# Optimization experiments

Measured on AMD Instinct MI355X. Metric: run time of the kernel, lower is better.

The kernel has to match this reference:

```python
import jax, jax.numpy as jnp
import numpy as np

B = 32          # num graphs
N = 4096        # nodes per graph (temporal length after reshape)
TOT = B * N     # 131072 total nodes
F = 64          # num_features
HS = 128        # hidden_dim_s
RS = 32         # rank_s
HT = 128        # hidden_dim_t
RT = 32         # rank_t
E = 1048576     # num edges


def setup_inputs() -> dict:
    key = jax.random.key(0)
    ks = jax.random.split(key, 20)
    x = jax.random.normal(ks[0], (TOT, F), jnp.float32)
    edge_index = jax.random.randint(ks[1], (2, E), 0, TOT, dtype=jnp.int64)
    batch = jnp.repeat(jnp.arange(B, dtype=jnp.int64), N)

    def lin(k, fan_in, fan_out):
        s = 1.0 / np.sqrt(fan_in)
        return jax.random.uniform(k, (fan_in, fan_out), jnp.float32, -s, s)

    def conv(k, cout, cin):
        s = 1.0 / np.sqrt(cin * 3)
        return jax.random.uniform(k, (cout, cin, 3), jnp.float32, -s, s)

    return {
        "x": x, "edge_index": edge_index, "batch": batch,
        "W1": lin(ks[2], F, HS), "b1": jnp.zeros((HS,), jnp.float32),
        "W2": lin(ks[3], HS, RS), "b2": jnp.zeros((RS,), jnp.float32),
        "W3": lin(ks[4], RS, HS), "b3": jnp.zeros((HS,), jnp.float32),
        "tW1": conv(ks[5], HT, HS), "tb1": jnp.zeros((HT,), jnp.float32),
        "tW2": conv(ks[6], RT, HT), "tb2": jnp.zeros((RT,), jnp.float32),
        "tW3": conv(ks[7], HT, RT), "tb3": jnp.zeros((HT,), jnp.float32),
        "Wpi": lin(ks[8], HT, 1), "bpi": jnp.zeros((1,), jnp.float32),
        "Wn": lin(ks[9], HT, 1), "bn": jnp.zeros((1,), jnp.float32),
        "Wp": lin(ks[10], HT, 1), "bp": jnp.zeros((1,), jnp.float32),
    }


def reference(x, edge_index, batch,
              W1, b1, W2, b2, W3, b3,
              tW1, tb1, tW2, tb2, tW3, tb3,
              Wpi, bpi, Wn, bn, Wp, bp):
    src, dst = edge_index[0], edge_index[1]
    n = x.shape[0]

    # GCN symmetric normalization with added self-loops (PyG GCNConv default)
    deg = jnp.zeros((n,), x.dtype).at[dst].add(1.0) + 1.0  # +1 self-loop
    dinv = jax.lax.rsqrt(deg)
    enorm = dinv[src] * dinv[dst]       # [E] edge normalization
    snorm = dinv * dinv                 # [n] self-loop normalization

    def gcn(h, W, b):
        h = h @ W                                            # [n, out]
        agg = jnp.zeros_like(h).at[dst].add(h[src] * enorm[:, None])
        return agg + h * snorm[:, None] + b

    xs = jax.nn.relu(gcn(x, W1, b1))
    xs = jax.nn.relu(gcn(xs, W2, b2))
    xs = jax.nn.relu(gcn(xs, W3, b3))    # [TOT, HS]

    num_graphs = B  # == batch.max() + 1 (batch is repeat(arange(B), N))
    xs = xs.reshape(num_graphs, -1, xs.shape[-1]).transpose(0, 2, 1)  # [B, HS, N]

    def conv1d(z, w, bias):
        y = jax.lax.conv_general_dilated(
            z, w, window_strides=(1,), padding=((1, 1),),
            dimension_numbers=("NCH", "OIH", "NCH"))
        return y + bias[None, :, None]

    xt = jax.nn.relu(conv1d(xs, tW1, tb1))
    xt = jax.nn.relu(conv1d(xt, tW2, tb2))
    xt = jax.nn.relu(conv1d(xt, tW3, tb3))                   # [B, HT, N]

    xt = xt.transpose(0, 2, 1).reshape(-1, xt.shape[1])      # [TOT, HT]

    pi = jax.nn.sigmoid(xt @ Wpi + bpi)
    nb = jax.nn.softplus(xt @ Wn + bn)
    p = jax.nn.sigmoid(xt @ Wp + bp)
    return (pi, nb, p)
```

## Files before the change

kernel.cpp:

```cpp
#include <hip/hip_runtime.h>
#include <cmath>

constexpr int TOT = 131072;
constexpr int NE  = 1048576;
constexpr int NMASK = 4095;

constexpr int NB   = 512;
constexpr int DPB  = 256;
constexpr int BCAP = 4096;
constexpr int EPB  = 2048;

typedef __attribute__((ext_vector_type(8))) short bf16x8;
typedef __attribute__((ext_vector_type(4))) float f32x4;

__device__ inline float bf2f(unsigned int u16) {
    union { unsigned int i; float f; } x; x.i = u16 << 16; return x.f;
}
__device__ inline unsigned short f2bf(float f) {
    union { float f; unsigned int i; } x; x.f = f;
    unsigned int r = (x.i + 0x7fffu + ((x.i >> 16) & 1u)) >> 16;
    return (unsigned short)r;
}
__device__ inline void unpack8(uint4 v, float* f) {
    f[0] = bf2f(v.x & 0xffffu); f[1] = bf2f(v.x >> 16);
    f[2] = bf2f(v.y & 0xffffu); f[3] = bf2f(v.y >> 16);
    f[4] = bf2f(v.z & 0xffffu); f[5] = bf2f(v.z >> 16);
    f[6] = bf2f(v.w & 0xffffu); f[7] = bf2f(v.w >> 16);
}
__device__ inline uint4 pack8(const float* f) {
    uint4 v;
    v.x = (unsigned)f2bf(f[0]) | ((unsigned)f2bf(f[1]) << 16);
    v.y = (unsigned)f2bf(f[2]) | ((unsigned)f2bf(f[3]) << 16);
    v.z = (unsigned)f2bf(f[4]) | ((unsigned)f2bf(f[5]) << 16);
    v.w = (unsigned)f2bf(f[6]) | ((unsigned)f2bf(f[7]) << 16);
    return v;
}

__global__ __launch_bounds__(256) void k_part(const int* __restrict__ src,
                                              const int* __restrict__ dst,
                                              int* __restrict__ gcur,
                                              unsigned* __restrict__ buf) {
    __shared__ int hist[NB];
    __shared__ int cbase[NB];
    __shared__ int lcur[NB];
    const int tid = threadIdx.x;
    const int e0 = blockIdx.x * EPB;

    for (int b = tid; b < NB; b += 256) hist[b] = 0;
    __syncthreads();
    for (int i = tid; i < EPB; i += 256)
        atomicAdd(&hist[dst[e0 + i] >> 8], 1);
    __syncthreads();
    for (int b = tid; b < NB; b += 256) {
        int c = hist[b];
        cbase[b] = (c > 0) ? atomicAdd(&gcur[b * 32], c) : 0;
        lcur[b] = 0;
    }
    __syncthreads();
    for (int i = tid; i < EPB; i += 256) {
        int e = e0 + i;
        int d = dst[e];
        int b = d >> 8;
        int p = atomicAdd(&lcur[b], 1);
        buf[b * BCAP + cbase[b] + p] = ((unsigned)src[e] << 8) | (unsigned)(d & 255);
    }
}

__global__ __launch_bounds__(256) void k_bcsr(const unsigned* __restrict__ buf,
                                              const int* __restrict__ gcur,
                                              int* __restrict__ adj,
                                              int2* __restrict__ rse,
                                              float* __restrict__ dinv) {
    __shared__ int cnt[DPB];
    __shared__ int start[DPB];
    __shared__ int cur[DPB];
    __shared__ int sc[DPB];
    const int b = blockIdx.x;
    const int tid = threadIdx.x;
    cnt[tid] = 0;
    __syncthreads();
    const int n = gcur[b * 32];
    const unsigned* eb = buf + b * BCAP;
    for (int i = tid; i < n; i += 256)
        atomicAdd(&cnt[eb[i] & 255u], 1);
    __syncthreads();
    int v = cnt[tid];
    sc[tid] = v;
    __syncthreads();
    for (int off = 1; off < 256; off <<= 1) {
        int a = sc[tid];
        int p = (tid >= off) ? sc[tid - off] : 0;
        __syncthreads();
        sc[tid] = a + p;
        __syncthreads();
    }
    int st = sc[tid] - v;
    start[tid] = st;
    cur[tid] = 0;
    int d = (b << 8) + tid;
    rse[d] = make_int2(b * BCAP + st, v);
    dinv[d] = rsqrtf((float)v + 1.0f);
    __syncthreads();
    for (int i = tid; i < n; i += 256) {
        unsigned w = eb[i];
        int dl = (int)(w & 255u);
        int p = atomicAdd(&cur[dl], 1);
        adj[b * BCAP + start[dl] + p] = (int)(w >> 8);
    }
}

__global__ __launch_bounds__(256) void k_packall(
    const float* __restrict__ W1, const float* __restrict__ W2, const float* __restrict__ W3,
    const float* __restrict__ tW1, const float* __restrict__ tW2, const float* __restrict__ tW3,
    unsigned short* __restrict__ g1, unsigned short* __restrict__ g2, unsigned short* __restrict__ g3,
    unsigned short* __restrict__ c1, unsigned short* __restrict__ c2, unsigned short* __restrict__ c3) {
    int gid = blockIdx.x * 256 + threadIdx.x;
    const float* w; unsigned short* wp; int CIN, COUT, taps, idx;
    if      (gid <  8192) { w = W1;  wp = g1; CIN = 64;  COUT = 128; taps = 1; idx = gid; }
    else if (gid < 12288) { w = W2;  wp = g2; CIN = 128; COUT = 32;  taps = 1; idx = gid - 8192; }
    else if (gid < 16384) { w = W3;  wp = g3; CIN = 32;  COUT = 128; taps = 1; idx = gid - 12288; }
    else if (gid < 65536) { w = tW1; wp = c1; CIN = 128; COUT = 128; taps = 3; idx = gid - 16384; }
    else if (gid < 77824) { w = tW2; wp = c2; CIN = 128; COUT = 32;  taps = 3; idx = gid - 65536; }
    else if (gid < 90112) { w = tW3; wp = c3; CIN = 32;  COUT = 128; taps = 3; idx = gid - 77824; }
    else return;
    int j = idx & 7;
    int L = (idx >> 3) & 63;
    int f = idx >> 9;
    int NT = COUT >> 4;
    int kc = f / NT, nt = f - kc * NT;
    int k = kc * 32 + (L >> 4) * 8 + j;
    int n = nt * 16 + (L & 15);
    float v;
    if (taps == 1) v = w[k * COUT + n];
    else { int t = k / CIN, c = k - t * CIN; v = w[(n * CIN + c) * 3 + t]; }
    wp[idx] = f2bf(v);
}

__global__ __launch_bounds__(256) void k_scale64b(const float4* __restrict__ x,
                                                  const float* __restrict__ dinv,
                                                  uint4* __restrict__ out) {
    int t = blockIdx.x * 256 + threadIdx.x;
    int row = t >> 3;
    float d = dinv[row];
    float4 v0 = x[t * 2], v1 = x[t * 2 + 1];
    float f[8] = { v0.x * d, v0.y * d, v0.z * d, v0.w * d,
                   v1.x * d, v1.y * d, v1.z * d, v1.w * d };
    out[t] = pack8(f);
}

template<int LC>
__global__ __launch_bounds__(256) void k_gcsr(const uint4* __restrict__ xs,
                                              const int* __restrict__ adj,
                                              const int2* __restrict__ rse,
                                              const float* __restrict__ dinv,
                                              const float* __restrict__ bias,
                                              uint4* __restrict__ out) {
    int t = blockIdx.x * 256 + threadIdx.x;
    int d = t >> LC;
    int g = t & ((1 << LC) - 1);
    float a[8];
    unpack8(xs[t], a);
    int2 se = rse[d];
    int e = se.x, end = se.x + se.y;
    for (; e + 4 <= end; e += 4) {
        int s0 = adj[e], s1 = adj[e + 1], s2 = adj[e + 2], s3 = adj[e + 3];
        uint4 v0 = xs[(s0 << LC) + g];
        uint4 v1 = xs[(s1 << LC) + g];
        uint4 v2 = xs[(s2 << LC) + g];
        uint4 v3 = xs[(s3 << LC) + g];
        float f[8];
        unpack8(v0, f);
#pragma unroll
        for (int j = 0; j < 8; ++j) a[j] += f[j];
        unpack8(v1, f);
#pragma unroll
        for (int j = 0; j < 8; ++j) a[j] += f[j];
        unpack8(v2, f);
#pragma unroll
        for (int j = 0; j < 8; ++j) a[j] += f[j];
        unpack8(v3, f);
#pragma unroll
        for (int j = 0; j < 8; ++j) a[j] += f[j];
    }
    for (; e < end; ++e) {
        float f[8];
        unpack8(xs[(adj[e] << LC) + g], f);
#pragma unroll
        for (int j = 0; j < 8; ++j) a[j] += f[j];
    }
    float dv = dinv[d];
#pragma unroll
    for (int j = 0; j < 8; ++j)
        a[j] = fmaxf(fmaf(a[j], dv, bias[g * 8 + j]), 0.0f) * dv;
    out[t] = pack8(a);
}

template<int CIN, bool RELU>
__global__ __launch_bounds__(256) void k_gmm(const uint4* __restrict__ xs,
                                             const int* __restrict__ adj,
                                             const int2* __restrict__ rse,
                                             const float* __restrict__ dinv,
                                             const bf16x8* __restrict__ wp,
                                             const float* __restrict__ bias,
                                             unsigned short* __restrict__ y) {
    constexpr int COUT = 128;
    constexpr int ROWS = 64;
    constexpr int SC = CIN + 8;
    constexpr int NV = CIN / 8;
    constexpr int VPT = NV / 4;
    constexpr int NK = CIN / 32;
    constexpr int NT = COUT / 16;
    constexpr int WN = 2, WM = 4;
    __shared__ __attribute__((aligned(16))) unsigned short tile[ROWS * SC];

    const int R0 = blockIdx.x * ROWS;
    const int tid = threadIdx.x;

    {
        int r = R0 + (tid >> 2);
        int g = tid & 3;
        const uint4* base = xs + (long)r * NV + g * VPT;
        float a[VPT * 8];
#pragma unroll
        for (int v = 0; v < VPT; ++v) unpack8(base[v], a + v * 8);
        int2 se = rse[r];
        int e = se.x, end = se.x + se.y;
        for (; e + 2 <= end; e += 2) {
            int s0 = adj[e], s1 = adj[e + 1];
            const uint4* p0 = xs + (long)s0 * NV + g * VPT;
            const uint4* p1 = xs + (long)s1 * NV + g * VPT;
            uint4 v0[VPT], v1[VPT];
#pragma unroll
            for (int v = 0; v < VPT; ++v) { v0[v] = p0[v]; v1[v] = p1[v]; }
            float f[VPT * 8];
#pragma unroll
            for (int v = 0; v < VPT; ++v) unpack8(v0[v], f + v * 8);
#pragma unroll
            for (int j = 0; j < VPT * 8; ++j) a[j] += f[j];
#pragma unroll
            for (int v = 0; v < VPT; ++v) unpack8(v1[v], f + v * 8);
#pragma unroll
            for (int j = 0; j < VPT * 8; ++j) a[j] += f[j];
        }
        for (; e < end; ++e) {
            const uint4* p0 = xs + (long)adj[e] * NV + g * VPT;
            float f[VPT * 8];
#pragma unroll
            for (int v = 0; v < VPT; ++v) unpack8(p0[v], f + v * 8);
#pragma unroll
            for (int j = 0; j < VPT * 8; ++j) a[j] += f[j];
        }
        float dv = dinv[r];
#pragma unroll
        for (int j = 0; j < VPT * 8; ++j) a[j] *= dv;
        uint4* dst4 = (uint4*)(tile + (tid >> 2) * SC + g * VPT * 8);
#pragma unroll
        for (int v = 0; v < VPT; ++v) dst4[v] = pack8(a + v * 8);
    }
    __syncthreads();

    const int lane = threadIdx.x & 63;
    const int w = threadIdx.x >> 6;
    const int l16 = lane & 15;
    const int q = lane >> 4;
    const int colbase = w * 32;
    const int nt0 = colbase >> 4;

    f32x4 acc[WM][WN];
#pragma unroll
    for (int wm = 0; wm < WM; ++wm)
#pragma unroll
        for (int nt = 0; nt < WN; ++nt) acc[wm][nt] = (f32x4){0.f, 0.f, 0.f, 0.f};

    const bf16x8* __restrict__ wpl = wp + lane;

#pragma unroll
    for (int kc = 0; kc < NK; ++kc) {
        bf16x8 a[WM];
#pragma unroll
        for (int wm = 0; wm < WM; ++wm)
            a[wm] = *(const bf16x8*)(tile + (wm * 16 + l16) * SC + kc * 32 + q * 8);
        bf16x8 b[WN];
#pragma unroll
        for (int nt = 0; nt < WN; ++nt)
            b[nt] = wpl[(kc * NT + nt0 + nt) * 64];
#pragma unroll
        for (int wm = 0; wm < WM; ++wm)
#pragma unroll
            for (int nt = 0; nt < WN; ++nt)
                acc[wm][nt] = __builtin_amdgcn_mfma_f32_16x16x32_bf16(a[wm], b[nt], acc[wm][nt], 0, 0, 0);
    }

#pragma unroll
    for (int wm = 0; wm < WM; ++wm) {
#pragma unroll
        for (int nt = 0; nt < WN; ++nt) {
            int col = colbase + nt * 16 + l16;
            float bi = bias[col];
#pragma unroll
            for (int r = 0; r < 4; ++r) {
                int row = R0 + wm * 16 + q * 4 + r;
                float v = acc[wm][nt][r] + bi;
                if (RELU) v = fmaxf(v, 0.0f);
                y[(long)row * COUT + col] = f2bf(v);
            }
        }
    }
}

template<int CIN, int COUT, int TAPS, bool RELU, bool BIAS, bool SOUT>
__global__ __launch_bounds__(256) void k_mm(const unsigned short* __restrict__ x,
                                            const bf16x8* __restrict__ wp,
                                            const float* __restrict__ bias,
                                            const float* __restrict__ dinv,
                                            unsigned short* __restrict__ y) {
    constexpr int ROWS = 64;
    constexpr int HALO = (TAPS == 3) ? 1 : 0;
    constexpr int TR = ROWS + 2 * HALO;
    constexpr int SC = CIN + 8;
    constexpr int NCH = CIN / 32;
    constexpr int NK = TAPS * NCH;
    constexpr int NT = COUT / 16;
    constexpr int WN = (COUT == 128) ? 2 : 1;
    constexpr int WM = (COUT == 128) ? 4 : 2;
    __shared__ __attribute__((aligned(16))) unsigned short tile[TR * SC];

    const int R0 = blockIdx.x * ROWS;
    const int n0 = R0 & NMASK; (void)n0;

    constexpr int NLD = TR * (CIN / 8);
    for (int idx = threadIdx.x; idx < NLD; idx += 256) {
        int tr = idx / (CIN / 8);
        int c8 = idx - tr * (CIN / 8);
        int ro = tr - HALO;
        bool valid = true;
        if (TAPS == 3) {
            if (ro < 0) valid = (n0 > 0);
            else if (ro >= ROWS) valid = (n0 + ROWS < 4096);
        }
        uint4 v = make_uint4(0, 0, 0, 0);
        if (valid) v = *(const uint4*)(x + (long)(R0 + ro) * CIN + c8 * 8);
        *(uint4*)(tile + tr * SC + c8 * 8) = v;
    }
    __syncthreads();

    const int lane = threadIdx.x & 63;
    const int w = threadIdx.x >> 6;
    const int l16 = lane & 15;
    const int q = lane >> 4;
    const int colbase = (COUT == 128) ? w * 32 : (w & 1) * 16;
    const int rowbase = (COUT == 128) ? 0 : (w >> 1) * 32;
    const int nt0 = colbase >> 4;

    f32x4 acc[WM][WN];
#pragma unroll
    for (int wm = 0; wm < WM; ++wm)
#pragma unroll
        for (int nt = 0; nt < WN; ++nt) acc[wm][nt] = (f32x4){0.f, 0.f, 0.f, 0.f};

    const bf16x8* __restrict__ wpl = wp + lane;

#pragma unroll
    for (int kc = 0; kc < NK; ++kc) {
        const int tap = (TAPS == 3) ? (kc / NCH) : 0;
        const int ch  = (TAPS == 3) ? (kc - tap * NCH) : kc;
        bf16x8 a[WM];
#pragma unroll
        for (int wm = 0; wm < WM; ++wm)
            a[wm] = *(const bf16x8*)(tile + (rowbase + wm * 16 + l16 + tap) * SC + ch * 32 + q * 8);
        bf16x8 b[WN];
#pragma unroll
        for (int nt = 0; nt < WN; ++nt)
            b[nt] = wpl[(kc * NT + nt0 + nt) * 64];
#pragma unroll
        for (int wm = 0; wm < WM; ++wm)
#pragma unroll
            for (int nt = 0; nt < WN; ++nt)
                acc[wm][nt] = __builtin_amdgcn_mfma_f32_16x16x32_bf16(a[wm], b[nt], acc[wm][nt], 0, 0, 0);
    }

#pragma unroll
    for (int wm = 0; wm < WM; ++wm) {
#pragma unroll
        for (int nt = 0; nt < WN; ++nt) {
            int col = colbase + nt * 16 + l16;
            float bi = BIAS ? bias[col] : 0.0f;
#pragma unroll
            for (int r = 0; r < 4; ++r) {
                int row = R0 + rowbase + wm * 16 + q * 4 + r;
                float v = acc[wm][nt][r] + bi;
                if (RELU) v = fmaxf(v, 0.0f);
                if (SOUT) v *= dinv[row];
                y[(long)row * COUT + col] = f2bf(v);
            }
        }
    }
}

__global__ __launch_bounds__(256) void k_conv_heads(
    const unsigned short* __restrict__ x, const bf16x8* __restrict__ wp,
    const float* __restrict__ bias,
    const float* __restrict__ Wpi, const float* __restrict__ bpi,
    const float* __restrict__ Wn,  const float* __restrict__ bn,
    const float* __restrict__ Wp,  const float* __restrict__ bp,
    float* __restrict__ out) {
    constexpr int CIN = 32;
    constexpr int ROWS = 64, HALO = 1, TR = 66, SC = CIN + 8;
    constexpr int NK = 3, NT = 8, WN = 2, WM = 4;
    __shared__ __attribute__((aligned(16))) unsigned short tile[TR * SC];
    __shared__ unsigned short xts[64 * 130];

    const int R0 = blockIdx.x * ROWS;
    const int n0 = R0 & NMASK;

    constexpr int NLD = TR * (CIN / 8);
    for (int idx = threadIdx.x; idx < NLD; idx += 256) {
        int tr = idx / (CIN / 8);
        int c8 = idx - tr * (CIN / 8);
        int ro = tr - HALO;
        bool valid = true;
        if (ro < 0) valid = (n0 > 0);
        else if (ro >= ROWS) valid = (n0 + ROWS < 4096);
        uint4 v = make_uint4(0, 0, 0, 0);
        if (valid) v = *(const uint4*)(x + (long)(R0 + ro) * CIN + c8 * 8);
        *(uint4*)(tile + tr * SC + c8 * 8) = v;
    }
    __syncthreads();

    const int lane = threadIdx.x & 63;
    const int w = threadIdx.x >> 6;
    const int l16 = lane & 15;
    const int q = lane >> 4;
    const int colbase = w * 32;
    const int nt0 = colbase >> 4;

    f32x4 acc[WM][WN];
#pragma unroll
    for (int wm = 0; wm < WM; ++wm)
#pragma unroll
        for (int nt = 0; nt < WN; ++nt) acc[wm][nt] = (f32x4){0.f, 0.f, 0.f, 0.f};

    const bf16x8* __restrict__ wpl = wp + lane;

#pragma unroll
    for (int kc = 0; kc < NK; ++kc) {
        bf16x8 a[WM];
#pragma unroll
        for (int wm = 0; wm < WM; ++wm)
            a[wm] = *(const bf16x8*)(tile + (wm * 16 + l16 + kc) * SC + q * 8);
        bf16x8 b[WN];
#pragma unroll
        for (int nt = 0; nt < WN; ++nt)
            b[nt] = wpl[(kc * NT + nt0 + nt) * 64];
#pragma unroll
        for (int wm = 0; wm < WM; ++wm)
#pragma unroll
            for (int nt = 0; nt < WN; ++nt)
                acc[wm][nt] = __builtin_amdgcn_mfma_f32_16x16x32_bf16(a[wm], b[nt], acc[wm][nt], 0, 0, 0);
    }

#pragma unroll
    for (int wm = 0; wm < WM; ++wm) {
#pragma unroll
        for (int nt = 0; nt < WN; ++nt) {
            int col = colbase + nt * 16 + l16;
            float bi = bias[col];
#pragma unroll
            for (int r = 0; r < 4; ++r) {
                int row = wm * 16 + q * 4 + r;
                xts[row * 130 + col] = f2bf(fmaxf(acc[wm][nt][r] + bi, 0.0f));
            }
        }
    }
    __syncthreads();
    if (threadIdx.x < 192) {
        int h = threadIdx.x >> 6;
        int row = threadIdx.x & 63;
        const float* Wh = (h == 0) ? Wpi : (h == 1) ? Wn : Wp;
        float s = 0.0f;
        const unsigned short* xr = xts + row * 130;
#pragma unroll
        for (int c2 = 0; c2 < 64; ++c2) {
            unsigned u = *(const unsigned*)(xr + c2 * 2);
            s = fmaf(bf2f(u & 0xffffu), Wh[c2 * 2], s);
            s = fmaf(bf2f(u >> 16), Wh[c2 * 2 + 1], s);
        }
        float bb = (h == 0) ? bpi[0] : (h == 1) ? bn[0] : bp[0];
        float z = s + bb;
        float o;
        if (h == 1) o = (z > 20.0f) ? z : log1pf(expf(z));
        else        o = 1.0f / (1.0f + expf(-z));
        out[h * TOT + R0 + row] = o;
    }
}

extern "C" void kernel_launch(void* const* d_in, const int* in_sizes, int n_in,
                              void* d_out, int out_size, void* d_ws, size_t ws_size,
                              hipStream_t stream) {
    const float* x   = (const float*)d_in[0];
    const int*   ei  = (const int*)d_in[1];
    const int*   src = ei;
    const int*   dst = ei + NE;
    const float* W1 = (const float*)d_in[3];
    const float* b1 = (const float*)d_in[4];
    const float* W2 = (const float*)d_in[5];
    const float* b2 = (const float*)d_in[6];
    const float* W3 = (const float*)d_in[7];
    const float* b3 = (const float*)d_in[8];
    const float* tW1 = (const float*)d_in[9];
    const float* tb1 = (const float*)d_in[10];
    const float* tW2 = (const float*)d_in[11];
    const float* tb2 = (const float*)d_in[12];
    const float* tW3 = (const float*)d_in[13];
    const float* tb3 = (const float*)d_in[14];
    const float* Wpi = (const float*)d_in[15];
    const float* bpi = (const float*)d_in[16];
    const float* Wn  = (const float*)d_in[17];
    const float* bn  = (const float*)d_in[18];
    const float* Wp  = (const float*)d_in[19];
    const float* bp  = (const float*)d_in[20];

    char* ws = (char*)d_ws;
    float* dinv = (float*)(ws + (0ull << 20));
    int*   gcur = (int*)  (ws + (1ull << 20));
    int2*  rse  = (int2*) (ws + (1ull << 20) + (256 << 10));
    unsigned short* wpG1 = (unsigned short*)(ws + (3ull << 20));
    unsigned short* wpG2 = (unsigned short*)(ws + (3ull << 20) + (128 << 10));
    unsigned short* wpG3 = (unsigned short*)(ws + (3ull << 20) + (256 << 10));
    unsigned short* wpC1 = (unsigned short*)(ws + (3ull << 20) + (384 << 10));
    unsigned short* wpC2 = (unsigned short*)(ws + (3ull << 20) + (512 << 10));
    unsigned short* wpC3 = (unsigned short*)(ws + (3ull << 20) + (640 << 10));
    unsigned* buf = (unsigned*)(ws + (4ull << 20));
    int* adj = (int*)(ws + (12ull << 20));
    unsigned short* Xa = (unsigned short*)(ws + (24ull  << 20));
    unsigned short* Xb = (unsigned short*)(ws + (44ull  << 20));
    unsigned short* Xc = (unsigned short*)(ws + (80ull  << 20));
    unsigned short* Xd = (unsigned short*)(ws + (116ull << 20));
    unsigned short* Xe = (unsigned short*)(ws + (128ull << 20));

    hipMemsetAsync(gcur, 0, NB * 32 * sizeof(int), stream);
    k_packall<<<352, 256, 0, stream>>>(W1, W2, W3, tW1, tW2, tW3,
                                       wpG1, wpG2, wpG3, wpC1, wpC2, wpC3);

    k_part<<<NE / EPB, 256, 0, stream>>>(src, dst, gcur, buf);
    k_bcsr<<<NB, 256, 0, stream>>>(buf, gcur, adj, rse, dinv);

    k_scale64b<<<TOT * 8 / 256, 256, 0, stream>>>((const float4*)x, dinv, (uint4*)Xa);
    k_gmm<64, true><<<TOT / 64, 256, 0, stream>>>((const uint4*)Xa, adj, rse, dinv,
                                                  (const bf16x8*)wpG1, b1, Xc);

    k_mm<128, 32, 1, false, false, true>
        <<<TOT / 64, 256, 0, stream>>>(Xc, (const bf16x8*)wpG2, nullptr, dinv, Xd);
    k_gcsr<2><<<TOT * 4 / 256, 256, 0, stream>>>((const uint4*)Xd, adj, rse, dinv,
                                                 b2, (uint4*)Xe);

    k_gmm<32, true><<<TOT / 64, 256, 0, stream>>>((const uint4*)Xe, adj, rse, dinv,
                                                  (const bf16x8*)wpG3, b3, Xb);

    k_mm<128, 128, 3, true, true, false>
        <<<TOT / 64, 256, 0, stream>>>(Xb, (const bf16x8*)wpC1, tb1, nullptr, Xc);
    k_mm<128, 32, 3, true, true, false>
        <<<TOT / 64, 256, 0, stream>>>(Xc, (const bf16x8*)wpC2, tb2, nullptr, Xd);

    k_conv_heads<<<TOT / 64, 256, 0, stream>>>(Xd, (const bf16x8*)wpC3, tb3,
                                               Wpi, bpi, Wn, bn, Wp, bp, (float*)d_out);
}
```

Measured before the change: 286.7 us.

## Fuse three temporal convs and heads into one halo-recompute kernel

Merges the three temporal conv1d layers and the output heads into a single kernel. Each block loads a 64-row tile with a 3-row halo and recomputes the halo rows of the intermediate layers in shared memory, so the intermediate activations are never written to or read from global memory. It also folds the input scaling into the CSR-build kernel to remove one launch, and unrolls the GCN gather loop by four. The cost is redundant halo compute, much larger shared memory per block (lower occupancy), and higher register pressure.

After: 288.0 us. About the same (+0.5%).

```diff
diff --git a/kernel.cpp b/kernel.cpp
--- a/kernel.cpp
+++ b/kernel.cpp
@@ -70,7 +70,9 @@
                                               const int* __restrict__ gcur,
                                               int* __restrict__ adj,
                                               int2* __restrict__ rse,
-                                              float* __restrict__ dinv) {
+                                              float* __restrict__ dinv,
+                                              const float4* __restrict__ x,
+                                              uint4* __restrict__ xsc) {
     __shared__ int cnt[DPB];
     __shared__ int start[DPB];
     __shared__ int cur[DPB];
@@ -106,6 +108,15 @@
         int dl = (int)(w & 255u);
         int p = atomicAdd(&cur[dl], 1);
         adj[b * BCAP + start[dl] + p] = (int)(w >> 8);
+    }
+    for (int i = tid; i < DPB * 8; i += 256) {
+        int rl = i >> 3;
+        int t = (b << 11) + i;
+        float dv = rsqrtf((float)cnt[rl] + 1.0f);
+        float4 v0 = x[t * 2], v1 = x[t * 2 + 1];
+        float f[8] = { v0.x * dv, v0.y * dv, v0.z * dv, v0.w * dv,
+                       v1.x * dv, v1.y * dv, v1.z * dv, v1.w * dv };
+        xsc[t] = pack8(f);
     }
 }
 
@@ -136,18 +147,6 @@
     wp[idx] = f2bf(v);
 }
 
-__global__ __launch_bounds__(256) void k_scale64b(const float4* __restrict__ x,
-                                                  const float* __restrict__ dinv,
-                                                  uint4* __restrict__ out) {
-    int t = blockIdx.x * 256 + threadIdx.x;
-    int row = t >> 3;
-    float d = dinv[row];
-    float4 v0 = x[t * 2], v1 = x[t * 2 + 1];
-    float f[8] = { v0.x * d, v0.y * d, v0.z * d, v0.w * d,
-                   v1.x * d, v1.y * d, v1.z * d, v1.w * d };
-    out[t] = pack8(f);
-}
-
 template<int LC>
 __global__ __launch_bounds__(256) void k_gcsr(const uint4* __restrict__ xs,
                                               const int* __restrict__ adj,
@@ -225,13 +224,15 @@
         for (int v = 0; v < VPT; ++v) unpack8(base[v], a + v * 8);
         int2 se = rse[r];
         int e = se.x, end = se.x + se.y;
-        for (; e + 2 <= end; e += 2) {
-            int s0 = adj[e], s1 = adj[e + 1];
+        for (; e + 4 <= end; e += 4) {
+            int s0 = adj[e], s1 = adj[e + 1], s2 = adj[e + 2], s3 = adj[e + 3];
             const uint4* p0 = xs + (long)s0 * NV + g * VPT;
             const uint4* p1 = xs + (long)s1 * NV + g * VPT;
-            uint4 v0[VPT], v1[VPT];
-#pragma unroll
-            for (int v = 0; v < VPT; ++v) { v0[v] = p0[v]; v1[v] = p1[v]; }
+            const uint4* p2 = xs + (long)s2 * NV + g * VPT;
+            const uint4* p3 = xs + (long)s3 * NV + g * VPT;
+            uint4 v0[VPT], v1[VPT], v2[VPT], v3[VPT];
+#pragma unroll
+            for (int v = 0; v < VPT; ++v) { v0[v] = p0[v]; v1[v] = p1[v]; v2[v] = p2[v]; v3[v] = p3[v]; }
             float f[VPT * 8];
 #pragma unroll
             for (int v = 0; v < VPT; ++v) unpack8(v0[v], f + v * 8);
@@ -239,6 +240,14 @@
             for (int j = 0; j < VPT * 8; ++j) a[j] += f[j];
 #pragma unroll
             for (int v = 0; v < VPT; ++v) unpack8(v1[v], f + v * 8);
+#pragma unroll
+            for (int j = 0; j < VPT * 8; ++j) a[j] += f[j];
+#pragma unroll
+            for (int v = 0; v < VPT; ++v) unpack8(v2[v], f + v * 8);
+#pragma unroll
+            for (int j = 0; j < VPT * 8; ++j) a[j] += f[j];
+#pragma unroll
+            for (int v = 0; v < VPT; ++v) unpack8(v3[v], f + v * 8);
 #pragma unroll
             for (int j = 0; j < VPT * 8; ++j) a[j] += f[j];
         }
@@ -308,38 +317,25 @@
     }
 }
 
-template<int CIN, int COUT, int TAPS, bool RELU, bool BIAS, bool SOUT>
+template<int CIN, int COUT, bool SOUT>
 __global__ __launch_bounds__(256) void k_mm(const unsigned short* __restrict__ x,
                                             const bf16x8* __restrict__ wp,
-                                            const float* __restrict__ bias,
                                             const float* __restrict__ dinv,
                                             unsigned short* __restrict__ y) {
     constexpr int ROWS = 64;
-    constexpr int HALO = (TAPS == 3) ? 1 : 0;
-    constexpr int TR = ROWS + 2 * HALO;
     constexpr int SC = CIN + 8;
-    constexpr int NCH = CIN / 32;
-    constexpr int NK = TAPS * NCH;
+    constexpr int NK = CIN / 32;
     constexpr int NT = COUT / 16;
-    constexpr int WN = (COUT == 128) ? 2 : 1;
-    constexpr int WM = (COUT == 128) ? 4 : 2;
-    __shared__ __attribute__((aligned(16))) unsigned short tile[TR * SC];
+    constexpr int WN = 1, WM = 2;
+    __shared__ __attribute__((aligned(16))) unsigned short tile[ROWS * SC];
 
     const int R0 = blockIdx.x * ROWS;
-    const int n0 = R0 & NMASK; (void)n0;
-
-    constexpr int NLD = TR * (CIN / 8);
+
+    constexpr int NLD = ROWS * (CIN / 8);
     for (int idx = threadIdx.x; idx < NLD; idx += 256) {
         int tr = idx / (CIN / 8);
         int c8 = idx - tr * (CIN / 8);
-        int ro = tr - HALO;
-        bool valid = true;
-        if (TAPS == 3) {
-            if (ro < 0) valid = (n0 > 0);
-            else if (ro >= ROWS) valid = (n0 + ROWS < 4096);
-        }
-        uint4 v = make_uint4(0, 0, 0, 0);
-        if (valid) v = *(const uint4*)(x + (long)(R0 + ro) * CIN + c8 * 8);
+        uint4 v = *(const uint4*)(x + (long)(R0 + tr) * CIN + c8 * 8);
         *(uint4*)(tile + tr * SC + c8 * 8) = v;
     }
     __syncthreads();
@@ -348,8 +344,8 @@
     const int w = threadIdx.x >> 6;
     const int l16 = lane & 15;
     const int q = lane >> 4;
-    const int colbase = (COUT == 128) ? w * 32 : (w & 1) * 16;
-    const int rowbase = (COUT == 128) ? 0 : (w >> 1) * 32;
+    const int colbase = (w & 1) * 16;
+    const int rowbase = (w >> 1) * 32;
     const int nt0 = colbase >> 4;
 
     f32x4 acc[WM][WN];
@@ -362,12 +358,10 @@
 
 #pragma unroll
     for (int kc = 0; kc < NK; ++kc) {
-        const int tap = (TAPS == 3) ? (kc / NCH) : 0;
-        const int ch  = (TAPS == 3) ? (kc - tap * NCH) : kc;
         bf16x8 a[WM];
 #pragma unroll
         for (int wm = 0; wm < WM; ++wm)
-            a[wm] = *(const bf16x8*)(tile + (rowbase + wm * 16 + l16 + tap) * SC + ch * 32 + q * 8);
+            a[wm] = *(const bf16x8*)(tile + (rowbase + wm * 16 + l16) * SC + kc * 32 + q * 8);
         bf16x8 b[WN];
 #pragma unroll
         for (int nt = 0; nt < WN; ++nt)
@@ -384,12 +378,10 @@
 #pragma unroll
         for (int nt = 0; nt < WN; ++nt) {
             int col = colbase + nt * 16 + l16;
-            float bi = BIAS ? bias[col] : 0.0f;
 #pragma unroll
             for (int r = 0; r < 4; ++r) {
                 int row = R0 + rowbase + wm * 16 + q * 4 + r;
-                float v = acc[wm][nt][r] + bi;
-                if (RELU) v = fmaxf(v, 0.0f);
+                float v = acc[wm][nt][r];
                 if (SOUT) v *= dinv[row];
                 y[(long)row * COUT + col] = f2bf(v);
             }
@@ -397,93 +389,173 @@
     }
 }
 
-__global__ __launch_bounds__(256) void k_conv_heads(
-    const unsigned short* __restrict__ x, const bf16x8* __restrict__ wp,
-    const float* __restrict__ bias,
+__global__ __launch_bounds__(256) void k_tconv_heads(
+    const unsigned short* __restrict__ x,
+    const bf16x8* __restrict__ wp1, const float* __restrict__ tb1,
+    const bf16x8* __restrict__ wp2, const float* __restrict__ tb2,
+    const bf16x8* __restrict__ wp3, const float* __restrict__ tb3,
     const float* __restrict__ Wpi, const float* __restrict__ bpi,
     const float* __restrict__ Wn,  const float* __restrict__ bn,
     const float* __restrict__ Wp,  const float* __restrict__ bp,
     float* __restrict__ out) {
-    constexpr int CIN = 32;
-    constexpr int ROWS = 64, HALO = 1, TR = 66, SC = CIN + 8;
-    constexpr int NK = 3, NT = 8, WN = 2, WM = 4;
-    __shared__ __attribute__((aligned(16))) unsigned short tile[TR * SC];
-    __shared__ unsigned short xts[64 * 130];
-
-    const int R0 = blockIdx.x * ROWS;
+    constexpr int SC1 = 136;
+    constexpr int SC2 = 40;
+    __shared__ __attribute__((aligned(16))) unsigned short shl[82 * 136 * 2 + 66 * 40];
+    unsigned short* xin = shl;
+    unsigned short* c1  = shl + 82 * 136;
+    unsigned short* c2  = shl + 2 * 82 * 136;
+    unsigned short* xts = shl;
+
+    const int R0 = blockIdx.x * 64;
     const int n0 = R0 & NMASK;
-
-    constexpr int NLD = TR * (CIN / 8);
-    for (int idx = threadIdx.x; idx < NLD; idx += 256) {
-        int tr = idx / (CIN / 8);
-        int c8 = idx - tr * (CIN / 8);
-        int ro = tr - HALO;
-        bool valid = true;
-        if (ro < 0) valid = (n0 > 0);
-        else if (ro >= ROWS) valid = (n0 + ROWS < 4096);
+    const int tid = threadIdx.x;
+
+    for (int i = tid; i < 82 * 16; i += 256) {
+        int r = i >> 4;
+        int c8 = i & 15;
+        int n = n0 - 3 + r;
         uint4 v = make_uint4(0, 0, 0, 0);
-        if (valid) v = *(const uint4*)(x + (long)(R0 + ro) * CIN + c8 * 8);
-        *(uint4*)(tile + tr * SC + c8 * 8) = v;
-    }
-    __syncthreads();
-
-    const int lane = threadIdx.x & 63;
-    const int w = threadIdx.x >> 6;
+        if (n >= 0 && n < 4096)
+            v = *(const uint4*)(x + (long)(R0 - 3 + r) * 128 + c8 * 8);
+        *(uint4*)(xin + r * SC1 + c8 * 8) = v;
+    }
+    for (int i = tid; i < 2 * 16; i += 256)
+        *(uint4*)(c1 + (80 + (i >> 4)) * SC1 + (i & 15) * 8) = make_uint4(0, 0, 0, 0);
+    __syncthreads();
+
+    const int lane = tid & 63;
+    const int w = tid >> 6;
     const int l16 = lane & 15;
     const int q = lane >> 4;
-    const int colbase = w * 32;
-    const int nt0 = colbase >> 4;
-
-    f32x4 acc[WM][WN];
-#pragma unroll
-    for (int wm = 0; wm < WM; ++wm)
-#pragma unroll
-        for (int nt = 0; nt < WN; ++nt) acc[wm][nt] = (f32x4){0.f, 0.f, 0.f, 0.f};
-
-    const bf16x8* __restrict__ wpl = wp + lane;
-
-#pragma unroll
-    for (int kc = 0; kc < NK; ++kc) {
-        bf16x8 a[WM];
-#pragma unroll
-        for (int wm = 0; wm < WM; ++wm)
-            a[wm] = *(const bf16x8*)(tile + (wm * 16 + l16 + kc) * SC + q * 8);
-        bf16x8 b[WN];
-#pragma unroll
-        for (int nt = 0; nt < WN; ++nt)
-            b[nt] = wpl[(kc * NT + nt0 + nt) * 64];
-#pragma unroll
-        for (int wm = 0; wm < WM; ++wm)
-#pragma unroll
-            for (int nt = 0; nt < WN; ++nt)
-                acc[wm][nt] = __builtin_amdgcn_mfma_f32_16x16x32_bf16(a[wm], b[nt], acc[wm][nt], 0, 0, 0);
-    }
-
-#pragma unroll
-    for (int wm = 0; wm < WM; ++wm) {
-#pragma unroll
-        for (int nt = 0; nt < WN; ++nt) {
-            int col = colbase + nt * 16 + l16;
-            float bi = bias[col];
+
+    {
+        f32x4 acc[5][2];
+#pragma unroll
+        for (int rt = 0; rt < 5; ++rt)
+#pragma unroll
+            for (int nt = 0; nt < 2; ++nt) acc[rt][nt] = (f32x4){0.f, 0.f, 0.f, 0.f};
+        const bf16x8* wpl = wp1 + lane;
+#pragma unroll
+        for (int kc = 0; kc < 12; ++kc) {
+            int tap = kc >> 2, ch = kc & 3;
+            bf16x8 a[5];
+#pragma unroll
+            for (int rt = 0; rt < 5; ++rt)
+                a[rt] = *(const bf16x8*)(xin + (16 * rt + l16 + tap) * SC1 + ch * 32 + q * 8);
+            bf16x8 b[2];
+#pragma unroll
+            for (int nt = 0; nt < 2; ++nt)
+                b[nt] = wpl[(kc * 8 + 2 * w + nt) * 64];
+#pragma unroll
+            for (int rt = 0; rt < 5; ++rt)
+#pragma unroll
+                for (int nt = 0; nt < 2; ++nt)
+                    acc[rt][nt] = __builtin_amdgcn_mfma_f32_16x16x32_bf16(a[rt], b[nt], acc[rt][nt], 0, 0, 0);
+        }
+#pragma unroll
+        for (int rt = 0; rt < 5; ++rt) {
+#pragma unroll
+            for (int nt = 0; nt < 2; ++nt) {
+                int col = w * 32 + nt * 16 + l16;
+                float bi = tb1[col];
+#pragma unroll
+                for (int r = 0; r < 4; ++r) {
+                    int idx = 16 * rt + q * 4 + r;
+                    int n = n0 - 2 + idx;
+                    unsigned short v = 0;
+                    if (n >= 0 && n < 4096)
+                        v = f2bf(fmaxf(acc[rt][nt][r] + bi, 0.0f));
+                    c1[idx * SC1 + col] = v;
+                }
+            }
+        }
+    }
+    __syncthreads();
+
+    for (int rt = w; rt < 5; rt += 4) {
+        f32x4 acc[2];
+#pragma unroll
+        for (int nt = 0; nt < 2; ++nt) acc[nt] = (f32x4){0.f, 0.f, 0.f, 0.f};
+        const bf16x8* wpl = wp2 + lane;
+#pragma unroll
+        for (int kc = 0; kc < 12; ++kc) {
+            int tap = kc >> 2, ch = kc & 3;
+            bf16x8 a = *(const bf16x8*)(c1 + (16 * rt + l16 + tap) * SC1 + ch * 32 + q * 8);
+            bf16x8 b0 = wpl[(kc * 2 + 0) * 64];
+            bf16x8 b1 = wpl[(kc * 2 + 1) * 64];
+            acc[0] = __builtin_amdgcn_mfma_f32_16x16x32_bf16(a, b0, acc[0], 0, 0, 0);
+            acc[1] = __builtin_amdgcn_mfma_f32_16x16x32_bf16(a, b1, acc[1], 0, 0, 0);
+        }
+#pragma unroll
+        for (int nt = 0; nt < 2; ++nt) {
+            int col = nt * 16 + l16;
+            float bi = tb2[col];
 #pragma unroll
             for (int r = 0; r < 4; ++r) {
-                int row = wm * 16 + q * 4 + r;
-                xts[row * 130 + col] = f2bf(fmaxf(acc[wm][nt][r] + bi, 0.0f));
+                int idx = 16 * rt + q * 4 + r;
+                if (idx < 66) {
+                    int n = n0 - 1 + idx;
+                    unsigned short v = 0;
+                    if (n >= 0 && n < 4096)
+                        v = f2bf(fmaxf(acc[nt][r] + bi, 0.0f));
+                    c2[idx * SC2 + col] = v;
+                }
             }
         }
     }
     __syncthreads();
-    if (threadIdx.x < 192) {
-        int h = threadIdx.x >> 6;
-        int row = threadIdx.x & 63;
+
+    {
+        f32x4 acc[4][2];
+#pragma unroll
+        for (int rt = 0; rt < 4; ++rt)
+#pragma unroll
+            for (int nt = 0; nt < 2; ++nt) acc[rt][nt] = (f32x4){0.f, 0.f, 0.f, 0.f};
+        const bf16x8* wpl = wp3 + lane;
+#pragma unroll
+        for (int kc = 0; kc < 3; ++kc) {
+            bf16x8 a[4];
+#pragma unroll
+            for (int rt = 0; rt < 4; ++rt)
+                a[rt] = *(const bf16x8*)(c2 + (16 * rt + l16 + kc) * SC2 + q * 8);
+            bf16x8 b[2];
+#pragma unroll
+            for (int nt = 0; nt < 2; ++nt)
+                b[nt] = wpl[(kc * 8 + 2 * w + nt) * 64];
+#pragma unroll
+            for (int rt = 0; rt < 4; ++rt)
+#pragma unroll
+                for (int nt = 0; nt < 2; ++nt)
+                    acc[rt][nt] = __builtin_amdgcn_mfma_f32_16x16x32_bf16(a[rt], b[nt], acc[rt][nt], 0, 0, 0);
+        }
+        __syncthreads();
+#pragma unroll
+        for (int rt = 0; rt < 4; ++rt) {
+#pragma unroll
+            for (int nt = 0; nt < 2; ++nt) {
+                int col = w * 32 + nt * 16 + l16;
+                float bi = tb3[col];
+#pragma unroll
+                for (int r = 0; r < 4; ++r) {
+                    int row = 16 * rt + q * 4 + r;
+                    xts[row * 130 + col] = f2bf(fmaxf(acc[rt][nt][r] + bi, 0.0f));
+                }
+            }
+        }
+    }
+    __syncthreads();
+
+    if (tid < 192) {
+        int h = tid >> 6;
+        int row = tid & 63;
         const float* Wh = (h == 0) ? Wpi : (h == 1) ? Wn : Wp;
         float s = 0.0f;
         const unsigned short* xr = xts + row * 130;
 #pragma unroll
-        for (int c2 = 0; c2 < 64; ++c2) {
-            unsigned u = *(const unsigned*)(xr + c2 * 2);
-            s = fmaf(bf2f(u & 0xffffu), Wh[c2 * 2], s);
-            s = fmaf(bf2f(u >> 16), Wh[c2 * 2 + 1], s);
+        for (int c2i = 0; c2i < 64; ++c2i) {
+            unsigned u = *(const unsigned*)(xr + c2i * 2);
+            s = fmaf(bf2f(u & 0xffffu), Wh[c2i * 2], s);
+            s = fmaf(bf2f(u >> 16), Wh[c2i * 2 + 1], s);
         }
         float bb = (h == 0) ? bpi[0] : (h == 1) ? bn[0] : bp[0];
         float z = s + bb;
@@ -543,25 +615,21 @@
                                        wpG1, wpG2, wpG3, wpC1, wpC2, wpC3);
 
     k_part<<<NE / EPB, 256, 0, stream>>>(src, dst, gcur, buf);
-    k_bcsr<<<NB, 256, 0, stream>>>(buf, gcur, adj, rse, dinv);
-
-    k_scale64b<<<TOT * 8 / 256, 256, 0, stream>>>((const float4*)x, dinv, (uint4*)Xa);
+    k_bcsr<<<NB, 256, 0, stream>>>(buf, gcur, adj, rse, dinv, (const float4*)x, (uint4*)Xa);
+
     k_gmm<64, true><<<TOT / 64, 256, 0, stream>>>((const uint4*)Xa, adj, rse, dinv,
                                                   (const bf16x8*)wpG1, b1, Xc);
 
-    k_mm<128, 32, 1, false, false, true>
-        <<<TOT / 64, 256, 0, stream>>>(Xc, (const bf16x8*)wpG2, nullptr, dinv, Xd);
+    k_mm<128, 32, true><<<TOT / 64, 256, 0, stream>>>(Xc, (const bf16x8*)wpG2, dinv, Xd);
     k_gcsr<2><<<TOT * 4 / 256, 256, 0, stream>>>((const uint4*)Xd, adj, rse, dinv,
                                                  b2, (uint4*)Xe);
 
     k_gmm<32, true><<<TOT / 64, 256, 0, stream>>>((const uint4*)Xe, adj, rse, dinv,
                                                   (const bf16x8*)wpG3, b3, Xb);
 
-    k_mm<128, 128, 3, true, true, false>
-        <<<TOT / 64, 256, 0, stream>>>(Xb, (const bf16x8*)wpC1, tb1, nullptr, Xc);
-    k_mm<128, 32, 3, true, true, false>
-        <<<TOT / 64, 256, 0, stream>>>(Xc, (const bf16x8*)wpC2, tb2, nullptr, Xd);
-
-    k_conv_heads<<<TOT / 64, 256, 0, stream>>>(Xd, (const bf16x8*)wpC3, tb3,
-                                               Wpi, bpi, Wn, bn, Wp, bp, (float*)d_out);
-}
+    k_tconv_heads<<<TOT / 64, 256, 0, stream>>>(Xb,
+                                                (const bf16x8*)wpC1, tb1,
+                                                (const bf16x8*)wpC2, tb2,
+                                                (const bf16x8*)wpC3, tb3,
+                                                Wpi, bpi, Wn, bn, Wp, bp, (float*)d_out);
+}
```
